# Optimization experiments

Measured on AMD Instinct MI355X. Metric: run time of the kernel, lower is better.

The kernel has to match this reference:

```python
import jax, jax.numpy as jnp
import numpy as np

BETA = 0.1
NBINS = 100
LM1 = float(np.log(0.01))   # lower histogram edge
LM2 = float(np.log(400.0))  # upper histogram edge
EPS = 1e-05


def _get_probability(x):
    # torch.histogram(x, 100, range=(lm1, lm2)): counts only in-range values,
    # right edge inclusive in last bin -- matches jnp.histogram semantics.
    h, _ = jnp.histogram(x.reshape(-1), bins=NBINS, range=(LM1, LM2))
    h = h.astype(jnp.float32) + EPS
    return h / jnp.sum(h)


def setup_inputs() -> dict:
    key = jax.random.key(0)
    k1, k2 = jax.random.split(key)
    shape = (128, 1, 512, 512)
    pred = jax.random.normal(k1, shape, dtype=jnp.float32)
    actual = jax.random.normal(k2, shape, dtype=jnp.float32)
    return {"pred": pred, "actual": actual}


def reference(pred, actual):
    # MSELoss(reduction='mean')
    mse = jnp.mean((pred - actual) ** 2)

    # KLDivLoss(reduction='batchmean', log_target=True) over 100-bin histograms;
    # input = log(p_pred), target = log(p_actual):
    #   sum(exp(t) * (t - i)) / N  with N = 100 (first dim of the histogram vec).
    p = _get_probability(pred)
    a = _get_probability(actual)
    kld = jnp.sum(a * (jnp.log(a) - jnp.log(p))) / NBINS

    return mse + BETA * kld
```

## Files before the change

kernel.cpp:

```cpp
#include <hip/hip_runtime.h>
#include <math.h>

#define NBINS 100
#define NCOPY 16
static constexpr float LM1f  = -4.605170185988091f;
static constexpr float LM2f  =  5.991464547107982f;
static constexpr float EPSV  = 1e-5f;
static constexpr float BETA  = 0.1f;

__global__ __launch_bounds__(256) void mse_hist_kernel(
    const float4* __restrict__ pred4, const float4* __restrict__ act4,
    const float* __restrict__ pred_s, const float* __restrict__ act_s,
    long long n,
    float* __restrict__ sumsq, unsigned int* __restrict__ hp,
    unsigned int* __restrict__ ha)
{
    __shared__ unsigned int sh[2 * NBINS * NCOPY];
    for (int i = threadIdx.x; i < 2 * NBINS * NCOPY; i += blockDim.x)
        sh[i] = 0u;
    __syncthreads();

    const int   c     = threadIdx.x & (NCOPY - 1);
    const float scale = (float)NBINS / (LM2f - LM1f);
    unsigned int* __restrict__ shp = sh;
    unsigned int* __restrict__ sha = sh + NBINS * NCOPY;

    float acc = 0.f;
    const long long n4 = n >> 2;
    const long long n8 = n4 >> 1;
    long long idx    = (long long)blockIdx.x * blockDim.x + threadIdx.x;
    long long stride = (long long)gridDim.x * blockDim.x;

#define HVAL(xv, base) do {                                       \
        float x_ = (xv);                                          \
        if (x_ >= LM1f && x_ <= LM2f) {                           \
            int b_ = (int)((x_ - LM1f) * scale);                  \
            if (b_ > NBINS - 1) b_ = NBINS - 1;                   \
            atomicAdd(&base[b_ * NCOPY + c], 1u);                 \
        }                                                         \
    } while (0)

    for (long long i = idx; i < n8; i += stride) {
        float4 p0 = pred4[2 * i];
        float4 p1 = pred4[2 * i + 1];
        float4 a0 = act4[2 * i];
        float4 a1 = act4[2 * i + 1];

        float d;
        d = p0.x - a0.x; acc += d * d;
        d = p0.y - a0.y; acc += d * d;
        d = p0.z - a0.z; acc += d * d;
        d = p0.w - a0.w; acc += d * d;
        d = p1.x - a1.x; acc += d * d;
        d = p1.y - a1.y; acc += d * d;
        d = p1.z - a1.z; acc += d * d;
        d = p1.w - a1.w; acc += d * d;

        HVAL(p0.x, shp); HVAL(p0.y, shp); HVAL(p0.z, shp); HVAL(p0.w, shp);
        HVAL(p1.x, shp); HVAL(p1.y, shp); HVAL(p1.z, shp); HVAL(p1.w, shp);
        HVAL(a0.x, sha); HVAL(a0.y, sha); HVAL(a0.z, sha); HVAL(a0.w, sha);
        HVAL(a1.x, sha); HVAL(a1.y, sha); HVAL(a1.z, sha); HVAL(a1.w, sha);
    }

    if (blockIdx.x == 0 && threadIdx.x == 0) {
        for (long long j = 2 * n8; j < n4; ++j) {
            float4 p = pred4[j], a = act4[j];
            float d;
            d = p.x - a.x; acc += d * d;
            d = p.y - a.y; acc += d * d;
            d = p.z - a.z; acc += d * d;
            d = p.w - a.w; acc += d * d;
            HVAL(p.x, shp); HVAL(p.y, shp); HVAL(p.z, shp); HVAL(p.w, shp);
            HVAL(a.x, sha); HVAL(a.y, sha); HVAL(a.z, sha); HVAL(a.w, sha);
        }
        for (long long j = 4 * n4; j < n; ++j) {
            float p = pred_s[j], a = act_s[j];
            float d = p - a; acc += d * d;
            HVAL(p, shp);
            HVAL(a, sha);
        }
    }
#undef HVAL
    __syncthreads();

    for (int bin = threadIdx.x; bin < 2 * NBINS; bin += blockDim.x) {
        unsigned int s = 0;
        const unsigned int* p = sh + bin * NCOPY;
        #pragma unroll
        for (int k = 0; k < NCOPY; ++k) s += p[k];
        if (s) {
            if (bin < NBINS) atomicAdd(&hp[bin], s);
            else             atomicAdd(&ha[bin - NBINS], s);
        }
    }

    for (int off = 32; off > 0; off >>= 1)
        acc += __shfl_down(acc, off);
    __shared__ float wsum[4];
    if ((threadIdx.x & 63) == 0) wsum[threadIdx.x >> 6] = acc;
    __syncthreads();
    if (threadIdx.x == 0)
        atomicAdd(sumsq, wsum[0] + wsum[1] + wsum[2] + wsum[3]);
}

__global__ __launch_bounds__(128) void finalize_kernel(
    const float* __restrict__ sumsq, const unsigned int* __restrict__ hp,
    const unsigned int* __restrict__ ha, float* __restrict__ out, float n_elems)
{
    const int t = threadIdx.x;
    float hpv = 0.f, hav = 0.f;
    if (t < NBINS) {
        hpv = (float)hp[t] + EPSV;
        hav = (float)ha[t] + EPSV;
    }

    float sp = hpv, sa = hav;
    for (int off = 32; off > 0; off >>= 1) {
        sp += __shfl_down(sp, off);
        sa += __shfl_down(sa, off);
    }
    __shared__ float shp[2], sha[2];
    if ((t & 63) == 0) { shp[t >> 6] = sp; sha[t >> 6] = sa; }
    __syncthreads();
    const float tot_p = shp[0] + shp[1];
    const float tot_a = sha[0] + sha[1];

    float term = 0.f;
    if (t < NBINS) {
        float pv = hpv / tot_p;
        float av = hav / tot_a;
        term = av * (logf(av) - logf(pv));
    }
    for (int off = 32; off > 0; off >>= 1)
        term += __shfl_down(term, off);
    __shared__ float st[2];
    if ((t & 63) == 0) st[t >> 6] = term;
    __syncthreads();
    if (t == 0) {
        float kld = (st[0] + st[1]) / (float)NBINS;
        out[0] = sumsq[0] / n_elems + BETA * kld;
    }
}

extern "C" void kernel_launch(void* const* d_in, const int* in_sizes, int n_in,
                              void* d_out, int out_size, void* d_ws, size_t ws_size,
                              hipStream_t stream) {
    const float* pred = (const float*)d_in[0];
    const float* act  = (const float*)d_in[1];
    const long long n = (long long)in_sizes[0];

    float*        sumsq = (float*)d_ws;
    unsigned int* hp    = (unsigned int*)d_ws + 1;
    unsigned int* ha    = (unsigned int*)d_ws + 1 + NBINS;

    hipMemsetAsync(d_ws, 0, (1 + 2 * NBINS) * sizeof(unsigned int), stream);

    const int blocks = 2048;
    mse_hist_kernel<<<blocks, 256, 0, stream>>>(
        (const float4*)pred, (const float4*)act, pred, act, n,
        sumsq, hp, ha);

    finalize_kernel<<<1, 128, 0, stream>>>(sumsq, hp, ha, (float*)d_out, (float)n);
}
```

Baseline: 94.20 us.

## Replace shared-memory atomic histograms with per-thread byte-packed private histograms

Each thread now keeps its own histogram of 8-bit counters packed four per dword in LDS (51 dwords per thread). Bins are bumped with plain adds instead of LDS atomics, and out-of-range values use a branchless zero increment. A strided cross-thread pass then sums the counters with SWAR 16-bit lane arithmetic and shuffles before the global atomics. The grid is halved so each thread's counters stay below 256 for this input size. The cost is a much larger LDS footprint per block, which may limit occupancy, and byte counters that would overflow if a thread processed more elements.

```diff
diff --git a/kernel.cpp b/kernel.cpp
--- a/kernel.cpp
+++ b/kernel.cpp
@@ -2,7 +2,7 @@
 #include <math.h>
 
 #define NBINS 100
-#define NCOPY 16
+#define STRIDE_DW 51
 static constexpr float LM1f  = -4.605170185988091f;
 static constexpr float LM2f  =  5.991464547107982f;
 static constexpr float EPSV  = 1e-5f;
@@ -15,30 +15,30 @@
     float* __restrict__ sumsq, unsigned int* __restrict__ hp,
     unsigned int* __restrict__ ha)
 {
-    __shared__ unsigned int sh[2 * NBINS * NCOPY];
-    for (int i = threadIdx.x; i < 2 * NBINS * NCOPY; i += blockDim.x)
-        sh[i] = 0u;
+    __shared__ unsigned int sh[256 * STRIDE_DW];
+    const int tid = threadIdx.x;
+    unsigned int* __restrict__ my = sh + tid * STRIDE_DW;
+    #pragma unroll
+    for (int i = 0; i < STRIDE_DW; ++i) my[i] = 0u;
     __syncthreads();
 
-    const int   c     = threadIdx.x & (NCOPY - 1);
     const float scale = (float)NBINS / (LM2f - LM1f);
-    unsigned int* __restrict__ shp = sh;
-    unsigned int* __restrict__ sha = sh + NBINS * NCOPY;
+
+#define BUMP(xv, off) do {                                                \
+        float x_ = (xv);                                                  \
+        int b_ = (int)((x_ - LM1f) * scale);                              \
+        b_ = b_ < 0 ? 0 : (b_ > NBINS - 1 ? NBINS - 1 : b_);              \
+        int byte_ = (off) + b_;                                           \
+        unsigned int inc_ =                                               \
+            (x_ >= LM1f && x_ <= LM2f) ? (1u << ((byte_ & 3) * 8)) : 0u;  \
+        my[byte_ >> 2] += inc_;                                           \
+    } while (0)
 
     float acc = 0.f;
     const long long n4 = n >> 2;
     const long long n8 = n4 >> 1;
-    long long idx    = (long long)blockIdx.x * blockDim.x + threadIdx.x;
+    long long idx    = (long long)blockIdx.x * blockDim.x + tid;
     long long stride = (long long)gridDim.x * blockDim.x;
-
-#define HVAL(xv, base) do {                                       \
-        float x_ = (xv);                                          \
-        if (x_ >= LM1f && x_ <= LM2f) {                           \
-            int b_ = (int)((x_ - LM1f) * scale);                  \
-            if (b_ > NBINS - 1) b_ = NBINS - 1;                   \
-            atomicAdd(&base[b_ * NCOPY + c], 1u);                 \
-        }                                                         \
-    } while (0)
 
     for (long long i = idx; i < n8; i += stride) {
         float4 p0 = pred4[2 * i];
@@ -56,50 +56,60 @@
         d = p1.z - a1.z; acc += d * d;
         d = p1.w - a1.w; acc += d * d;
 
-        HVAL(p0.x, shp); HVAL(p0.y, shp); HVAL(p0.z, shp); HVAL(p0.w, shp);
-        HVAL(p1.x, shp); HVAL(p1.y, shp); HVAL(p1.z, shp); HVAL(p1.w, shp);
-        HVAL(a0.x, sha); HVAL(a0.y, sha); HVAL(a0.z, sha); HVAL(a0.w, sha);
-        HVAL(a1.x, sha); HVAL(a1.y, sha); HVAL(a1.z, sha); HVAL(a1.w, sha);
+        BUMP(p0.x, 0); BUMP(p0.y, 0); BUMP(p0.z, 0); BUMP(p0.w, 0);
+        BUMP(p1.x, 0); BUMP(p1.y, 0); BUMP(p1.z, 0); BUMP(p1.w, 0);
+        BUMP(a0.x, NBINS); BUMP(a0.y, NBINS); BUMP(a0.z, NBINS); BUMP(a0.w, NBINS);
+        BUMP(a1.x, NBINS); BUMP(a1.y, NBINS); BUMP(a1.z, NBINS); BUMP(a1.w, NBINS);
     }
 
-    if (blockIdx.x == 0 && threadIdx.x == 0) {
-        for (long long j = 2 * n8; j < n4; ++j) {
-            float4 p = pred4[j], a = act4[j];
-            float d;
-            d = p.x - a.x; acc += d * d;
-            d = p.y - a.y; acc += d * d;
-            d = p.z - a.z; acc += d * d;
-            d = p.w - a.w; acc += d * d;
-            HVAL(p.x, shp); HVAL(p.y, shp); HVAL(p.z, shp); HVAL(p.w, shp);
-            HVAL(a.x, sha); HVAL(a.y, sha); HVAL(a.z, sha); HVAL(a.w, sha);
-        }
-        for (long long j = 4 * n4; j < n; ++j) {
+    if (blockIdx.x == 0 && tid == 0) {
+        for (long long j = 8 * n8; j < n; ++j) {
             float p = pred_s[j], a = act_s[j];
             float d = p - a; acc += d * d;
-            HVAL(p, shp);
-            HVAL(a, sha);
+            BUMP(p, 0);
+            BUMP(a, NBINS);
         }
     }
-#undef HVAL
+#undef BUMP
     __syncthreads();
 
-    for (int bin = threadIdx.x; bin < 2 * NBINS; bin += blockDim.x) {
-        unsigned int s = 0;
-        const unsigned int* p = sh + bin * NCOPY;
+    if (tid < 4 * (2 * NBINS / 4)) {
+        const int w = tid >> 2, q = tid & 3;
+        unsigned int accL = 0, accH = 0;
         #pragma unroll
-        for (int k = 0; k < NCOPY; ++k) s += p[k];
-        if (s) {
-            if (bin < NBINS) atomicAdd(&hp[bin], s);
-            else             atomicAdd(&ha[bin - NBINS], s);
+        for (int j = 0; j < 64; ++j) {
+            int jj = (j + 16 * q) & 63;
+            unsigned int v = sh[(64 * q + jj) * STRIDE_DW + w];
+            accL += v & 0x00FF00FFu;
+            accH += (v >> 8) & 0x00FF00FFu;
+        }
+        accL += __shfl_xor(accL, 1);
+        accH += __shfl_xor(accH, 1);
+        accL += __shfl_xor(accL, 2);
+        accH += __shfl_xor(accH, 2);
+        if (q == 0) {
+            unsigned int c[4];
+            c[0] = accL & 0xFFFFu;
+            c[1] = accH & 0xFFFFu;
+            c[2] = accL >> 16;
+            c[3] = accH >> 16;
+            #pragma unroll
+            for (int k = 0; k < 4; ++k) {
+                int B = 4 * w + k;
+                if (c[k]) {
+                    if (B < NBINS) atomicAdd(&hp[B], c[k]);
+                    else           atomicAdd(&ha[B - NBINS], c[k]);
+                }
+            }
         }
     }
 
     for (int off = 32; off > 0; off >>= 1)
         acc += __shfl_down(acc, off);
     __shared__ float wsum[4];
-    if ((threadIdx.x & 63) == 0) wsum[threadIdx.x >> 6] = acc;
+    if ((tid & 63) == 0) wsum[tid >> 6] = acc;
     __syncthreads();
-    if (threadIdx.x == 0)
+    if (tid == 0)
         atomicAdd(sumsq, wsum[0] + wsum[1] + wsum[2] + wsum[3]);
 }
 
@@ -155,7 +165,7 @@
 
     hipMemsetAsync(d_ws, 0, (1 + 2 * NBINS) * sizeof(unsigned int), stream);
 
-    const int blocks = 2048;
+    const int blocks = 1024;
     mse_hist_kernel<<<blocks, 256, 0, stream>>>(
         (const float4*)pred, (const float4*)act, pred, act, n,
         sumsq, hp, ha);
```

After: 132.8 us. +41.0%, slower.
